# Optimization experiments

Measured on AMD Instinct MI355X. Metric: run time of the kernel, lower is better.

## Reference

```python
import jax, jax.numpy as jnp
import numpy as np

B, N, M = 8, 1024, 1024
D_MODEL, D_HEAD, M_BITS = 1024, 128, 32
SCALE = 1.0 / np.sqrt(M_BITS)


def setup_inputs() -> dict:
    key = jax.random.key(0)
    ks = jax.random.split(key, 11)
    w_std = 1.0 / np.sqrt(D_MODEL)  # ~ nn.Linear init scale
    f32 = jnp.float32
    return {
        "Q": jax.random.normal(ks[0], (B, N, D_MODEL), dtype=f32),
        "K": jax.random.normal(ks[1], (B, M, D_MODEL), dtype=f32),
        "V": jax.random.normal(ks[2], (B, M, D_MODEL), dtype=f32),
        "Wq_boolean": jax.random.normal(ks[3], (D_MODEL, M_BITS), dtype=f32) * w_std,
        "Wk_boolean": jax.random.normal(ks[4], (D_MODEL, M_BITS), dtype=f32) * w_std,
        "Wq_tropical": jax.random.normal(ks[5], (D_MODEL, M_BITS), dtype=f32) * w_std,
        "Wk_tropical": jax.random.normal(ks[6], (D_MODEL, M_BITS), dtype=f32) * w_std,
        "Wq_real": jax.random.normal(ks[7], (D_MODEL, M_BITS), dtype=f32) * w_std,
        "Wk_real": jax.random.normal(ks[8], (D_MODEL, M_BITS), dtype=f32) * w_std,
        "Wv": jax.random.normal(ks[9], (D_MODEL, D_HEAD), dtype=f32) * w_std,
        "fusion_weights": jnp.ones((3,), dtype=f32),
        "mask": jnp.ones((B, N, M), dtype=jnp.int32),
    }


def _tropical_sim(Qe, Ke):
    # max-plus (tropical) witness similarity: sim[b,n,m] = max_d (Qe[b,n,d] + Ke[b,m,d])
    # loop over the small fixed bit dim (M_BITS=32) to avoid a [B,N,M,M_BITS] tensor
    acc = Qe[:, :, 0][:, :, None] + Ke[:, :, 0][:, None, :]
    for b in range(1, M_BITS):
        acc = jnp.maximum(acc, Qe[:, :, b][:, :, None] + Ke[:, :, b][:, None, :])
    return acc  # [B,N,M]


def reference(Q, K, V, Wq_boolean, Wk_boolean, Wq_tropical, Wk_tropical,
              Wq_real, Wk_real, Wv, fusion_weights, mask):
    # --- boolean monoid: hard-binarized codes, bit-match count ---
    Qb = (Q @ Wq_boolean > 0).astype(Q.dtype)   # [B,N,m]
    Kb = (K @ Wk_boolean > 0).astype(K.dtype)   # [B,M,m]
    sim_bool = (jnp.einsum('bnd,bmd->bnm', Qb, Kb)
                + jnp.einsum('bnd,bmd->bnm', 1.0 - Qb, 1.0 - Kb))
    # --- tropical monoid: max-plus over continuous codes ---
    sim_trop = _tropical_sim(Q @ Wq_tropical, K @ Wk_tropical)
    # --- real monoid: inner product of continuous codes ---
    sim_real = jnp.einsum('bnd,bmd->bnm', Q @ Wq_real, K @ Wk_real)
    # --- learned fusion + scaled softmax attention ---
    w = jax.nn.softmax(fusion_weights)
    scores = (w[0] * sim_bool + w[1] * sim_trop + w[2] * sim_real) * SCALE
    scores = jnp.where(mask == 0, -jnp.inf, scores)
    attn = jax.nn.softmax(scores, axis=-1)     # [B,N,M]  (dropout: eval mode, identity)
    out = jnp.einsum('bnm,bmh->bnh', attn, V @ Wv)  # [B,N,d_head]
    return out, attn
```

## Files before the change

kernel.cpp:

```cpp
#include <hip/hip_runtime.h>
#include <stdint.h>
#include <math.h>


#define SCALE_F 0.17677669529663687f

typedef float4 f4;

__device__ __forceinline__ float f4c(const f4 v, int i) {
    return i == 0 ? v.x : (i == 1 ? v.y : (i == 2 ? v.z : v.w));
}


__global__ __launch_bounds__(256)
void proj_qk_kernel(const float* __restrict__ Q, const float* __restrict__ K,
                    const float* __restrict__ Wqb, const float* __restrict__ Wkb,
                    const float* __restrict__ Wqt, const float* __restrict__ Wkt,
                    const float* __restrict__ Wqr, const float* __restrict__ Wkr,
                    float* __restrict__ Pq, float* __restrict__ Pk) {
    const int t = threadIdx.x;
    const int bx = blockIdx.x;
    const int by = blockIdx.y;
    const int side = blockIdx.z;
    const float* __restrict__ X  = side ? K   : Q;
    const float* __restrict__ Wb = side ? Wkb : Wqb;
    const float* __restrict__ Wt = side ? Wkt : Wqt;
    const float* __restrict__ Wr = side ? Wkr : Wqr;
    float* __restrict__ P = side ? Pk : Pq;

    __shared__ float Xs[128][68];
    __shared__ float Ws[64][96];

    const int r0 = bx * 128;
    const int rt = t >> 3;
    const int cg = t & 7;

    float acc[4][12];
    #pragma unroll
    for (int i = 0; i < 4; ++i)
        #pragma unroll
        for (int j = 0; j < 12; ++j) acc[i][j] = 0.f;

    for (int dc = 0; dc < 4; ++dc) {
        const int dbase = by * 256 + dc * 64;
        #pragma unroll
        for (int k2 = 0; k2 < 8; ++k2) {
            int idx = t + k2 * 256;
            int r = idx >> 4, c4 = idx & 15;
            *(f4*)&Xs[r][c4 * 4] = *(const f4*)&X[(size_t)(r0 + r) * 1024 + dbase + c4 * 4];
        }
        #pragma unroll
        for (int k2 = 0; k2 < 6; ++k2) {
            int idx = t + k2 * 256;
            int d = idx / 24, c4 = idx % 24;
            const float* __restrict__ src = (c4 < 8) ? Wb : ((c4 < 16) ? Wt : Wr);
            *(f4*)&Ws[d][c4 * 4] = *(const f4*)&src[(size_t)(dbase + d) * 32 + (c4 & 7) * 4];
        }
        __syncthreads();
        for (int dd = 0; dd < 64; dd += 4) {
            f4 xf[4];
            #pragma unroll
            for (int i = 0; i < 4; ++i) xf[i] = *(const f4*)&Xs[4 * rt + i][dd];
            #pragma unroll
            for (int d2 = 0; d2 < 4; ++d2) {
                f4 wf[3];
                #pragma unroll
                for (int jj = 0; jj < 3; ++jj)
                    wf[jj] = *(const f4*)&Ws[dd + d2][12 * cg + 4 * jj];
                #pragma unroll
                for (int i = 0; i < 4; ++i) {
                    const float xv = f4c(xf[i], d2);
                    #pragma unroll
                    for (int jj = 0; jj < 3; ++jj) {
                        acc[i][jj * 4 + 0] += xv * wf[jj].x;
                        acc[i][jj * 4 + 1] += xv * wf[jj].y;
                        acc[i][jj * 4 + 2] += xv * wf[jj].z;
                        acc[i][jj * 4 + 3] += xv * wf[jj].w;
                    }
                }
            }
        }
        __syncthreads();
    }
    #pragma unroll
    for (int i = 0; i < 4; ++i) {
        size_t base = ((size_t)by * 8192 + r0 + 4 * rt + i) * 96 + 12 * cg;
        *(f4*)&P[base + 0] = make_float4(acc[i][0], acc[i][1], acc[i][2],  acc[i][3]);
        *(f4*)&P[base + 4] = make_float4(acc[i][4], acc[i][5], acc[i][6],  acc[i][7]);
        *(f4*)&P[base + 8] = make_float4(acc[i][8], acc[i][9], acc[i][10], acc[i][11]);
    }
}

__global__ __launch_bounds__(256)
void proj_v_kernel(const float* __restrict__ V, const float* __restrict__ Wv,
                   float* __restrict__ P) {
    const int t = threadIdx.x;
    const int r0 = blockIdx.x * 128;
    const int by = blockIdx.y;
    __shared__ float Xs[128][36];
    __shared__ float Ws[32][128];
    const int rt = t >> 3, cg = t & 7;

    float acc[4][16];
    #pragma unroll
    for (int i = 0; i < 4; ++i)
        #pragma unroll
        for (int j = 0; j < 16; ++j) acc[i][j] = 0.f;

    for (int dc = 0; dc < 8; ++dc) {
        const int dbase = by * 256 + dc * 32;
        #pragma unroll
        for (int k2 = 0; k2 < 4; ++k2) {
            int idx = t + k2 * 256;
            int r = idx >> 3, c4 = idx & 7;
            *(f4*)&Xs[r][c4 * 4] = *(const f4*)&V[(size_t)(r0 + r) * 1024 + dbase + c4 * 4];
        }
        #pragma unroll
        for (int k2 = 0; k2 < 4; ++k2) {
            int idx = t + k2 * 256;
            int d = idx >> 5, c4 = idx & 31;
            *(f4*)&Ws[d][c4 * 4] = *(const f4*)&Wv[(size_t)(dbase + d) * 128 + c4 * 4];
        }
        __syncthreads();
        for (int dd = 0; dd < 32; dd += 4) {
            f4 xf[4];
            #pragma unroll
            for (int i = 0; i < 4; ++i) xf[i] = *(const f4*)&Xs[4 * rt + i][dd];
            #pragma unroll
            for (int d2 = 0; d2 < 4; ++d2) {
                f4 wf[4];
                #pragma unroll
                for (int jj = 0; jj < 4; ++jj)
                    wf[jj] = *(const f4*)&Ws[dd + d2][16 * cg + 4 * jj];
                #pragma unroll
                for (int i = 0; i < 4; ++i) {
                    const float xv = f4c(xf[i], d2);
                    #pragma unroll
                    for (int jj = 0; jj < 4; ++jj) {
                        acc[i][jj * 4 + 0] += xv * wf[jj].x;
                        acc[i][jj * 4 + 1] += xv * wf[jj].y;
                        acc[i][jj * 4 + 2] += xv * wf[jj].z;
                        acc[i][jj * 4 + 3] += xv * wf[jj].w;
                    }
                }
            }
        }
        __syncthreads();
    }
    #pragma unroll
    for (int i = 0; i < 4; ++i) {
        size_t base = ((size_t)by * 8192 + r0 + 4 * rt + i) * 128 + 16 * cg;
        #pragma unroll
        for (int jj = 0; jj < 4; ++jj)
            *(f4*)&P[base + 4 * jj] = make_float4(acc[i][jj * 4 + 0], acc[i][jj * 4 + 1],
                                                  acc[i][jj * 4 + 2], acc[i][jj * 4 + 3]);
    }
}


__global__ __launch_bounds__(256)
void pack_codes_kernel(const float* __restrict__ Pq, const float* __restrict__ Pk,
                       float* __restrict__ Qt, float* __restrict__ Qr,
                       float* __restrict__ Kt, float* __restrict__ Kr) {
    const int gid = blockIdx.x * 256 + threadIdx.x;
    const int side = blockIdx.y;
    const float* __restrict__ P = side ? Pk : Pq;
    const int row = gid >> 6, c = gid & 63;
    float s = 0.f;
    #pragma unroll
    for (int g = 0; g < 4; ++g) s += P[((size_t)g * 8192 + row) * 96 + 32 + c];
    float* __restrict__ dT = side ? Kt : Qt;
    float* __restrict__ dR = side ? Kr : Qr;
    if (c < 32) dT[row * 32 + c] = s;
    else        dR[row * 32 + (c - 32)] = s;
}

__global__ __launch_bounds__(256)
void pack_bits_kernel(const float* __restrict__ Pq, const float* __restrict__ Pk,
                      uint32_t* __restrict__ Qbits, uint32_t* __restrict__ Kbits) {
    const int gid = blockIdx.x * 256 + threadIdx.x;
    const int side = blockIdx.y;
    const float* __restrict__ P = side ? Pk : Pq;
    const int row = gid >> 5, c = gid & 31;
    float s = 0.f;
    #pragma unroll
    for (int g = 0; g < 4; ++g) s += P[((size_t)g * 8192 + row) * 96 + c];
    const unsigned long long bm = __ballot(s > 0.f);
    uint32_t* __restrict__ bits = side ? Kbits : Qbits;
    const int lane = threadIdx.x & 63;
    if (lane == 0)       bits[row] = (uint32_t)bm;
    else if (lane == 32) bits[row] = (uint32_t)(bm >> 32);
}

__global__ __launch_bounds__(256)
void reduce4_kernel(const float* __restrict__ P, float* __restrict__ dst) {
    const int gid = blockIdx.x * 256 + threadIdx.x;
    f4 a = ((const f4*)P)[gid];
    f4 b = ((const f4*)P)[262144 + gid];
    f4 c = ((const f4*)P)[2 * 262144 + gid];
    f4 d = ((const f4*)P)[3 * 262144 + gid];
    ((f4*)dst)[gid] = make_float4(a.x + b.x + c.x + d.x, a.y + b.y + c.y + d.y,
                                  a.z + b.z + c.z + d.z, a.w + b.w + c.w + d.w);
}


__global__ __launch_bounds__(256)
void scores_kernel(const float* __restrict__ Qt, const float* __restrict__ Qr,
                   const float* __restrict__ Kt, const float* __restrict__ Kr,
                   const uint32_t* __restrict__ Qbits, const uint32_t* __restrict__ Kbits,
                   const float* __restrict__ fw, float* __restrict__ attn) {
    const int t = threadIdx.x;
    const int m0 = blockIdx.x * 64;
    const int n0 = blockIdx.y * 64;
    const int b  = blockIdx.z;

    __shared__ float Qt_s[64][36], Qr_s[64][36];
    __shared__ float KtT[32][68],  KrT[32][68];
    __shared__ uint32_t qb_s[64], kb_s[64];

    #pragma unroll
    for (int k2 = 0; k2 < 2; ++k2) {
        int idx = t + k2 * 256;
        int r = idx >> 3, c4 = idx & 7;
        *(f4*)&Qt_s[r][c4 * 4] = *(const f4*)&Qt[(size_t)(b * 1024 + n0 + r) * 32 + c4 * 4];
        *(f4*)&Qr_s[r][c4 * 4] = *(const f4*)&Qr[(size_t)(b * 1024 + n0 + r) * 32 + c4 * 4];
        f4 vt = *(const f4*)&Kt[(size_t)(b * 1024 + m0 + r) * 32 + c4 * 4];
        f4 vr = *(const f4*)&Kr[(size_t)(b * 1024 + m0 + r) * 32 + c4 * 4];
        KtT[c4 * 4 + 0][r] = vt.x; KtT[c4 * 4 + 1][r] = vt.y;
        KtT[c4 * 4 + 2][r] = vt.z; KtT[c4 * 4 + 3][r] = vt.w;
        KrT[c4 * 4 + 0][r] = vr.x; KrT[c4 * 4 + 1][r] = vr.y;
        KrT[c4 * 4 + 2][r] = vr.z; KrT[c4 * 4 + 3][r] = vr.w;
    }
    if (t < 64)       qb_s[t] = Qbits[b * 1024 + n0 + t];
    else if (t < 128) kb_s[t - 64] = Kbits[b * 1024 + m0 + (t - 64)];
    __syncthreads();

    const float f0 = fw[0], f1 = fw[1], f2 = fw[2];
    const float fm = fmaxf(f0, fmaxf(f1, f2));
    const float e0 = __expf(f0 - fm), e1 = __expf(f1 - fm), e2 = __expf(f2 - fm);
    const float wi = 1.f / (e0 + e1 + e2);
    const float w0 = e0 * wi, w1 = e1 * wi, w2 = e2 * wi;

    const int rg = t >> 4, mg = t & 15;

    float tacc[4][4], racc[4][4];
    #pragma unroll
    for (int i = 0; i < 4; ++i)
        #pragma unroll
        for (int j = 0; j < 4; ++j) { tacc[i][j] = -INFINITY; racc[i][j] = 0.f; }

    for (int d0 = 0; d0 < 32; d0 += 4) {
        f4 qt4[4], qr4[4];
        #pragma unroll
        for (int i = 0; i < 4; ++i) {
            qt4[i] = *(const f4*)&Qt_s[4 * rg + i][d0];
            qr4[i] = *(const f4*)&Qr_s[4 * rg + i][d0];
        }
        #pragma unroll
        for (int d2 = 0; d2 < 4; ++d2) {
            const f4 kt = *(const f4*)&KtT[d0 + d2][4 * mg];
            const f4 kr = *(const f4*)&KrT[d0 + d2][4 * mg];
            #pragma unroll
            for (int i = 0; i < 4; ++i) {
                const float qtv = f4c(qt4[i], d2);
                const float qrv = f4c(qr4[i], d2);
                tacc[i][0] = fmaxf(tacc[i][0], qtv + kt.x);
                tacc[i][1] = fmaxf(tacc[i][1], qtv + kt.y);
                tacc[i][2] = fmaxf(tacc[i][2], qtv + kt.z);
                tacc[i][3] = fmaxf(tacc[i][3], qtv + kt.w);
                racc[i][0] += qrv * kr.x;
                racc[i][1] += qrv * kr.y;
                racc[i][2] += qrv * kr.z;
                racc[i][3] += qrv * kr.w;
            }
        }
    }

    uint32_t qb[4], kb[4];
    #pragma unroll
    for (int i = 0; i < 4; ++i) { qb[i] = qb_s[4 * rg + i]; kb[i] = kb_s[4 * mg + i]; }
    #pragma unroll
    for (int i = 0; i < 4; ++i) {
        float sj[4];
        #pragma unroll
        for (int j = 0; j < 4; ++j) {
            const float cnt = (float)(32 - __popc(qb[i] ^ kb[j]));
            sj[j] = (w0 * cnt + w1 * tacc[i][j] + w2 * racc[i][j]) * SCALE_F;
        }
        *(f4*)&attn[(size_t)(b * 1024 + n0 + 4 * rg + i) * 1024 + m0 + 4 * mg] =
            make_float4(sj[0], sj[1], sj[2], sj[3]);
    }
}


__global__ __launch_bounds__(256)
void softmax_kernel(float* __restrict__ attn, const int* __restrict__ mask) {
    const int row = blockIdx.x;
    const int t = threadIdx.x;
    const f4  s4 = ((const f4*)attn)[(size_t)row * 256 + t];
    const int4 m4 = ((const int4*)mask)[(size_t)row * 256 + t];
    const float v0 = m4.x ? s4.x : -INFINITY;
    const float v1 = m4.y ? s4.y : -INFINITY;
    const float v2 = m4.z ? s4.z : -INFINITY;
    const float v3 = m4.w ? s4.w : -INFINITY;

    float tm = fmaxf(fmaxf(v0, v1), fmaxf(v2, v3));
    #pragma unroll
    for (int off = 32; off >= 1; off >>= 1) tm = fmaxf(tm, __shfl_xor(tm, off, 64));
    __shared__ float rmax[4], rsum[4];
    if ((t & 63) == 0) rmax[t >> 6] = tm;
    __syncthreads();
    const float gm = fmaxf(fmaxf(rmax[0], rmax[1]), fmaxf(rmax[2], rmax[3]));

    const float x0 = m4.x ? __expf(v0 - gm) : 0.f;
    const float x1 = m4.y ? __expf(v1 - gm) : 0.f;
    const float x2 = m4.z ? __expf(v2 - gm) : 0.f;
    const float x3 = m4.w ? __expf(v3 - gm) : 0.f;
    float ts = (x0 + x1) + (x2 + x3);
    #pragma unroll
    for (int off = 32; off >= 1; off >>= 1) ts += __shfl_xor(ts, off, 64);
    if ((t & 63) == 0) rsum[t >> 6] = ts;
    __syncthreads();
    const float inv = 1.f / (((rsum[0] + rsum[1]) + (rsum[2] + rsum[3])));

    ((f4*)attn)[(size_t)row * 256 + t] = make_float4(x0 * inv, x1 * inv, x2 * inv, x3 * inv);
}


__global__ __launch_bounds__(256)
void pv_kernel(const float* __restrict__ attn, const float* __restrict__ Vp,
               float* __restrict__ Pout) {
    const int t = threadIdx.x;
    const int row0 = blockIdx.x * 64;
    const int ms = blockIdx.y;
    const int b = row0 >> 10;
    __shared__ float As[64][68];
    __shared__ float Vs[64][128];
    const int rt = t >> 4, hg = t & 15;

    float acc[4][8];
    #pragma unroll
    for (int i = 0; i < 4; ++i)
        #pragma unroll
        for (int j = 0; j < 8; ++j) acc[i][j] = 0.f;

    for (int mc = 0; mc < 4; ++mc) {
        const int mb = ms * 256 + mc * 64;
        #pragma unroll
        for (int k2 = 0; k2 < 4; ++k2) {
            int idx = t + k2 * 256;
            int r = idx >> 4, c4 = idx & 15;
            *(f4*)&As[r][c4 * 4] = *(const f4*)&attn[(size_t)(row0 + r) * 1024 + mb + c4 * 4];
        }
        #pragma unroll
        for (int k2 = 0; k2 < 8; ++k2) {
            int idx = t + k2 * 256;
            int m = idx >> 5, c4 = idx & 31;
            *(f4*)&Vs[m][c4 * 4] = *(const f4*)&Vp[(size_t)(b * 1024 + mb + m) * 128 + c4 * 4];
        }
        __syncthreads();
        for (int m = 0; m < 64; ++m) {
            const f4 u0 = *(const f4*)&Vs[m][hg * 8];
            const f4 u1 = *(const f4*)&Vs[m][hg * 8 + 4];
            #pragma unroll
            for (int i = 0; i < 4; ++i) {
                const float a = As[4 * rt + i][m];
                acc[i][0] += a * u0.x; acc[i][1] += a * u0.y;
                acc[i][2] += a * u0.z; acc[i][3] += a * u0.w;
                acc[i][4] += a * u1.x; acc[i][5] += a * u1.y;
                acc[i][6] += a * u1.z; acc[i][7] += a * u1.w;
            }
        }
        __syncthreads();
    }
    #pragma unroll
    for (int i = 0; i < 4; ++i) {
        size_t base = ((size_t)ms * 8192 + row0 + 4 * rt + i) * 128 + hg * 8;
        *(f4*)&Pout[base]     = make_float4(acc[i][0], acc[i][1], acc[i][2], acc[i][3]);
        *(f4*)&Pout[base + 4] = make_float4(acc[i][4], acc[i][5], acc[i][6], acc[i][7]);
    }
}


extern "C" void kernel_launch(void* const* d_in, const int* in_sizes, int n_in,
                              void* d_out, int out_size, void* d_ws, size_t ws_size,
                              hipStream_t stream) {
    const float* Q   = (const float*)d_in[0];
    const float* K   = (const float*)d_in[1];
    const float* V   = (const float*)d_in[2];
    const float* Wqb = (const float*)d_in[3];
    const float* Wkb = (const float*)d_in[4];
    const float* Wqt = (const float*)d_in[5];
    const float* Wkt = (const float*)d_in[6];
    const float* Wqr = (const float*)d_in[7];
    const float* Wkr = (const float*)d_in[8];
    const float* Wv  = (const float*)d_in[9];
    const float* fw  = (const float*)d_in[10];
    const int*  mask = (const int*)d_in[11];

    float* ws = (float*)d_ws;
    float* Qt = ws;
    float* Qr = Qt + 262144;
    float* Kt = Qr + 262144;
    float* Kr = Kt + 262144;
    float* Vp = Kr + 262144;
    uint32_t* Qbits = (uint32_t*)(Vp + 1048576);
    uint32_t* Kbits = Qbits + 8192;
    float* Pbig = (float*)(Kbits + 8192);

    float* out  = (float*)d_out;
    float* attn = out + 1048576;
    float* Pq = attn;
    float* Pk = attn + 3145728;

    proj_qk_kernel<<<dim3(64, 4, 2), 256, 0, stream>>>(Q, K, Wqb, Wkb, Wqt, Wkt, Wqr, Wkr, Pq, Pk);
    proj_v_kernel<<<dim3(64, 4), 256, 0, stream>>>(V, Wv, Pbig);
    pack_codes_kernel<<<dim3(2048, 2), 256, 0, stream>>>(Pq, Pk, Qt, Qr, Kt, Kr);
    pack_bits_kernel<<<dim3(1024, 2), 256, 0, stream>>>(Pq, Pk, Qbits, Kbits);
    reduce4_kernel<<<1024, 256, 0, stream>>>(Pbig, Vp);
    scores_kernel<<<dim3(16, 16, 8), 256, 0, stream>>>(Qt, Qr, Kt, Kr, Qbits, Kbits, fw, attn);
    softmax_kernel<<<8192, 256, 0, stream>>>(attn, mask);
    pv_kernel<<<dim3(128, 4), 256, 0, stream>>>(attn, Vp, Pbig);
    reduce4_kernel<<<1024, 256, 0, stream>>>(Pbig, out);
}
```

Baseline: 313.7 us.

## Rewrite pipeline on bf16 split-precision MFMA with packed f16 tropical max-plus

```diff
diff --git a/kernel.cpp b/kernel.cpp
--- a/kernel.cpp
+++ b/kernel.cpp
@@ -1,4 +1,5 @@
 #include <hip/hip_runtime.h>
+#include <hip/hip_fp16.h>
 #include <stdint.h>
 #include <math.h>
 
@@ -6,305 +7,377 @@
 #define SCALE_F 0.17677669529663687f
 
 typedef float4 f4;
-
+typedef unsigned int uint_t;
+typedef __attribute__((ext_vector_type(8))) short s16x8;
+typedef __attribute__((ext_vector_type(8))) unsigned short u16x8;
+typedef __attribute__((ext_vector_type(4))) float f32x4;
+
+__device__ __forceinline__ unsigned short f2bf(float x) {
+    unsigned u = __float_as_uint(x);
+    return (unsigned short)((u + 0x7FFFu + ((u >> 16) & 1u)) >> 16);
+}
+__device__ __forceinline__ float bf2f(unsigned short h) {
+    return __uint_as_float(((unsigned)h) << 16);
+}
 __device__ __forceinline__ float f4c(const f4 v, int i) {
     return i == 0 ? v.x : (i == 1 ? v.y : (i == 2 ? v.z : v.w));
 }
+__device__ __forceinline__ unsigned pk_add(unsigned a, unsigned b) {
+    unsigned r;
+    asm("v_pk_add_f16 %0, %1, %2" : "=v"(r) : "v"(a), "v"(b));
+    return r;
+}
+__device__ __forceinline__ unsigned pk_max(unsigned a, unsigned b) {
+    unsigned r;
+    asm("v_pk_max_f16 %0, %1, %2" : "=v"(r) : "v"(a), "v"(b));
+    return r;
+}
+__device__ __forceinline__ float h2f(unsigned short u) {
+    __half h;
+    *reinterpret_cast<unsigned short*>(&h) = u;
+    return __half2float(h);
+}
+__device__ __forceinline__ unsigned short f2h(float x) {
+    __half h = __float2half(x);
+    return *reinterpret_cast<unsigned short*>(&h);
+}
+
+#define MFMA16(a, b, c) __builtin_amdgcn_mfma_f32_16x16x32_bf16((a), (b), (c), 0, 0, 0)
 
 
 __global__ __launch_bounds__(256)
-void proj_qk_kernel(const float* __restrict__ Q, const float* __restrict__ K,
-                    const float* __restrict__ Wqb, const float* __restrict__ Wkb,
-                    const float* __restrict__ Wqt, const float* __restrict__ Wkt,
-                    const float* __restrict__ Wqr, const float* __restrict__ Wkr,
-                    float* __restrict__ Pq, float* __restrict__ Pk) {
+void conv_w_kernel(const float* __restrict__ Wqb, const float* __restrict__ Wkb,
+                   const float* __restrict__ Wqt, const float* __restrict__ Wkt,
+                   const float* __restrict__ Wqr, const float* __restrict__ Wkr,
+                   const float* __restrict__ Wv,
+                   unsigned short* __restrict__ Wh, unsigned short* __restrict__ Wm,
+                   unsigned short* __restrict__ Wl3,
+                   unsigned short* __restrict__ Wvh, unsigned short* __restrict__ Wvm) {
+    __shared__ float T[256][33];
     const int t = threadIdx.x;
+    const int bid = blockIdx.x;
+    const float* src;
+    int kb, outRowBase, srcStride, srcColBase, side = 0;
+    bool isQK, isBool;
+    if (bid < 24) {
+        side = bid / 12;
+        int cb = (bid % 12) / 4;
+        kb = bid & 3;
+        const float* mats[6] = {Wqb, Wqt, Wqr, Wkb, Wkt, Wkr};
+        src = mats[side * 3 + cb];
+        srcStride = 32; srcColBase = 0;
+        outRowBase = side * 96 + cb * 32;
+        isQK = true; isBool = (cb == 0);
+    } else {
+        int v = bid - 24;
+        int hb = v >> 2; kb = v & 3;
+        src = Wv; srcStride = 128; srcColBase = hb * 32;
+        outRowBase = hb * 32;
+        isQK = false; isBool = false;
+    }
+    #pragma unroll
+    for (int i = 0; i < 8; ++i) {
+        int idx = t + i * 256;
+        int r = idx >> 3, c4 = idx & 7;
+        f4 v = *(const f4*)&src[(size_t)(kb * 256 + r) * srcStride + srcColBase + c4 * 4];
+        T[r][c4 * 4 + 0] = v.x; T[r][c4 * 4 + 1] = v.y;
+        T[r][c4 * 4 + 2] = v.z; T[r][c4 * 4 + 3] = v.w;
+    }
+    __syncthreads();
+    const int col = t >> 3, kseg = t & 7;
+    unsigned short* dh = isQK ? Wh : Wvh;
+    unsigned short* dm = isQK ? Wm : Wvm;
+    size_t obase = (size_t)(outRowBase + col) * 1024 + kb * 256 + kseg * 32;
+    u16x8 ph[4], pm[4], pl[4];
+    #pragma unroll
+    for (int i = 0; i < 32; ++i) {
+        float x = T[kseg * 32 + i][col];
+        unsigned short hb_ = f2bf(x);
+        float r1 = x - bf2f(hb_);
+        unsigned short mb_ = f2bf(r1);
+        float r2 = r1 - bf2f(mb_);
+        ph[i >> 3][i & 7] = hb_;
+        pm[i >> 3][i & 7] = mb_;
+        pl[i >> 3][i & 7] = f2bf(r2);
+    }
+    #pragma unroll
+    for (int i = 0; i < 4; ++i) {
+        *(u16x8*)&dh[obase + i * 8] = ph[i];
+        *(u16x8*)&dm[obase + i * 8] = pm[i];
+    }
+    if (isBool) {
+        size_t lbase = (size_t)(side * 32 + col) * 1024 + kb * 256 + kseg * 32;
+        #pragma unroll
+        for (int i = 0; i < 4; ++i) *(u16x8*)&Wl3[lbase + i * 8] = pl[i];
+    }
+}
+
+
+__global__ __launch_bounds__(256)
+void proj_kernel(const float* __restrict__ Q, const float* __restrict__ K,
+                 const float* __restrict__ V,
+                 const unsigned short* __restrict__ Wh, const unsigned short* __restrict__ Wm,
+                 const unsigned short* __restrict__ Wl3,
+                 const unsigned short* __restrict__ Wvh, const unsigned short* __restrict__ Wvm,
+                 unsigned short* __restrict__ Qt_q, unsigned short* __restrict__ Kt_q,
+                 unsigned short* __restrict__ Qrh, unsigned short* __restrict__ Qrm,
+                 unsigned short* __restrict__ Krh, unsigned short* __restrict__ Krm,
+                 uint_t* __restrict__ Qbits, uint_t* __restrict__ Kbits,
+                 unsigned short* __restrict__ VphT, unsigned short* __restrict__ VpmT) {
+    __shared__ unsigned short BH[16384], BM[16384], BL[4096];
+    __shared__ uint_t sb[64];
+    const int t = threadIdx.x, lane = t & 63, w = t >> 6;
+    const int g = lane >> 4, l15 = lane & 15;
     const int bx = blockIdx.x;
-    const int by = blockIdx.y;
-    const int side = blockIdx.z;
-    const float* __restrict__ X  = side ? K   : Q;
-    const float* __restrict__ Wb = side ? Wkb : Wqb;
-    const float* __restrict__ Wt = side ? Wkt : Wqt;
-    const float* __restrict__ Wr = side ? Wkr : Wqr;
-    float* __restrict__ P = side ? Pk : Pq;
-
-    __shared__ float Xs[128][68];
-    __shared__ float Ws[64][96];
-
-    const int r0 = bx * 128;
-    const int rt = t >> 3;
-    const int cg = t & 7;
-
-    float acc[4][12];
-    #pragma unroll
-    for (int i = 0; i < 4; ++i)
-        #pragma unroll
-        for (int j = 0; j < 12; ++j) acc[i][j] = 0.f;
-
-    for (int dc = 0; dc < 4; ++dc) {
-        const int dbase = by * 256 + dc * 64;
-        #pragma unroll
-        for (int k2 = 0; k2 < 8; ++k2) {
-            int idx = t + k2 * 256;
-            int r = idx >> 4, c4 = idx & 15;
-            *(f4*)&Xs[r][c4 * 4] = *(const f4*)&X[(size_t)(r0 + r) * 1024 + dbase + c4 * 4];
-        }
-        #pragma unroll
-        for (int k2 = 0; k2 < 6; ++k2) {
-            int idx = t + k2 * 256;
-            int d = idx / 24, c4 = idx % 24;
-            const float* __restrict__ src = (c4 < 8) ? Wb : ((c4 < 16) ? Wt : Wr);
-            *(f4*)&Ws[d][c4 * 4] = *(const f4*)&src[(size_t)(dbase + d) * 32 + (c4 & 7) * 4];
+    const bool isV = bx >= 256;
+    const int side = isV ? 2 : (bx >> 7);
+    const int tile = isV ? (bx - 256) : (bx & 127);
+    const float* __restrict__ X = (side == 0) ? Q : (side == 1 ? K : V);
+    const int row0 = isV ? tile * 32 : tile * 64;
+    const int rowh = isV ? (w & 1) * 16 : w * 16;
+    const int hbase = isV ? (w >> 1) * 64 : 0;
+    const int arowg = row0 + rowh + l15;
+    const float* __restrict__ Xrow = X + (size_t)arowg * 1024;
+
+    if (t < 64) sb[t] = 0;
+
+    f32x4 acc[8];
+    #pragma unroll
+    for (int i = 0; i < 8; ++i) acc[i] = f32x4{0.f, 0.f, 0.f, 0.f};
+
+    for (int c = 0; c < 8; ++c) {
+        const int k0 = c * 128;
+        f4 ar[8];
+        #pragma unroll
+        for (int ks = 0; ks < 4; ++ks) {
+            ar[2 * ks]     = *(const f4*)&Xrow[k0 + ks * 32 + g * 8];
+            ar[2 * ks + 1] = *(const f4*)&Xrow[k0 + ks * 32 + g * 8 + 4];
         }
         __syncthreads();
-        for (int dd = 0; dd < 64; dd += 4) {
-            f4 xf[4];
-            #pragma unroll
-            for (int i = 0; i < 4; ++i) xf[i] = *(const f4*)&Xs[4 * rt + i][dd];
-            #pragma unroll
-            for (int d2 = 0; d2 < 4; ++d2) {
-                f4 wf[3];
+        if (!isV) {
+            #pragma unroll
+            for (int i = 0; i < 14; ++i) {
+                int s = t + i * 256;
+                int col, ks; const unsigned short* src; char* dp;
+                if (s < 1536)      { col = s >> 4; ks = s & 15;
+                    src = &Wh[(size_t)(side * 96 + col) * 1024 + k0 + ks * 8]; dp = (char*)BH; }
+                else if (s < 3072) { int s2 = s - 1536; col = s2 >> 4; ks = s2 & 15;
+                    src = &Wm[(size_t)(side * 96 + col) * 1024 + k0 + ks * 8]; dp = (char*)BM; }
+                else               { int s2 = s - 3072; col = s2 >> 4; ks = s2 & 15;
+                    src = &Wl3[(size_t)(side * 32 + col) * 1024 + k0 + ks * 8]; dp = (char*)BL; }
+                u16x8 v = *(const u16x8*)src;
+                *(u16x8*)(dp + col * 256 + ((ks * 16) ^ ((col & 7) << 4))) = v;
+            }
+        } else {
+            #pragma unroll
+            for (int i = 0; i < 16; ++i) {
+                int s = t + i * 256;
+                int col, ks; const unsigned short* src; char* dp;
+                if (s < 2048) { col = s >> 4; ks = s & 15;
+                    src = &Wvh[(size_t)col * 1024 + k0 + ks * 8]; dp = (char*)BH; }
+                else          { int s2 = s - 2048; col = s2 >> 4; ks = s2 & 15;
+                    src = &Wvm[(size_t)col * 1024 + k0 + ks * 8]; dp = (char*)BM; }
+                u16x8 v = *(const u16x8*)src;
+                *(u16x8*)(dp + col * 256 + ((ks * 16) ^ ((col & 7) << 4))) = v;
+            }
+        }
+        __syncthreads();
+
+        #pragma unroll
+        for (int ks = 0; ks < 4; ++ks) {
+            u16x8 ah, am, al;
+            #pragma unroll
+            for (int j = 0; j < 8; ++j) {
+                float x = (j < 4) ? f4c(ar[2 * ks], j) : f4c(ar[2 * ks + 1], j - 4);
+                unsigned short hb_ = f2bf(x);
+                float r1 = x - bf2f(hb_);
+                unsigned short mb_ = f2bf(r1);
+                ah[j] = hb_; am[j] = mb_;
+                al[j] = f2bf(r1 - bf2f(mb_));
+            }
+            s16x8 a1 = (s16x8)ah, a2 = (s16x8)am;
+            const int kbyte = (ks * 4 + g) * 16;
+            if (!isV) {
+                s16x8 a3 = (s16x8)al;
                 #pragma unroll
-                for (int jj = 0; jj < 3; ++jj)
-                    wf[jj] = *(const f4*)&Ws[dd + d2][12 * cg + 4 * jj];
+                for (int cf = 0; cf < 2; ++cf) {
+                    int col = cf * 16 + l15;
+                    int off = col * 256 + (kbyte ^ ((col & 7) << 4));
+                    s16x8 bh = *(s16x8*)((char*)BH + off);
+                    s16x8 bm = *(s16x8*)((char*)BM + off);
+                    s16x8 bl = *(s16x8*)((char*)BL + off);
+                    acc[cf] = MFMA16(a1, bh, acc[cf]);
+                    acc[cf] = MFMA16(a1, bm, acc[cf]);
+                    acc[cf] = MFMA16(a2, bh, acc[cf]);
+                    acc[cf] = MFMA16(a2, bm, acc[cf]);
+                    acc[cf] = MFMA16(a3, bh, acc[cf]);
+                }
                 #pragma unroll
-                for (int i = 0; i < 4; ++i) {
-                    const float xv = f4c(xf[i], d2);
+                for (int cf = 2; cf < 4; ++cf) {
+                    int col = cf * 16 + l15;
+                    int off = col * 256 + (kbyte ^ ((col & 7) << 4));
+                    s16x8 bh = *(s16x8*)((char*)BH + off);
+                    acc[cf] = MFMA16(a1, bh, acc[cf]);
+                }
+                #pragma unroll
+                for (int cf = 4; cf < 6; ++cf) {
+                    int col = cf * 16 + l15;
+                    int off = col * 256 + (kbyte ^ ((col & 7) << 4));
+                    s16x8 bh = *(s16x8*)((char*)BH + off);
+                    s16x8 bm = *(s16x8*)((char*)BM + off);
+                    acc[cf] = MFMA16(a1, bh, acc[cf]);
+                    acc[cf] = MFMA16(a1, bm, acc[cf]);
+                    acc[cf] = MFMA16(a2, bh, acc[cf]);
+                }
+            } else {
+                #pragma unroll
+                for (int cf = 0; cf < 4; ++cf) {
+                    int col = hbase + cf * 16 + l15;
+                    int off = col * 256 + (kbyte ^ ((col & 7) << 4));
+                    s16x8 bh = *(s16x8*)((char*)BH + off);
+                    s16x8 bm = *(s16x8*)((char*)BM + off);
+                    acc[cf] = MFMA16(a1, bh, acc[cf]);
+                    acc[cf] = MFMA16(a1, bm, acc[cf]);
+                    acc[cf] = MFMA16(a2, bh, acc[cf]);
+                }
+            }
+        }
+    }
+
+    if (!isV) {
+        #pragma unroll
+        for (int cf = 0; cf < 2; ++cf)
+            #pragma unroll
+            for (int r = 0; r < 4; ++r) {
+                unsigned long long bm = __ballot(acc[cf][r] > 0.f);
+                if (lane == 0) {
                     #pragma unroll
-                    for (int jj = 0; jj < 3; ++jj) {
-                        acc[i][jj * 4 + 0] += xv * wf[jj].x;
-                        acc[i][jj * 4 + 1] += xv * wf[jj].y;
-                        acc[i][jj * 4 + 2] += xv * wf[jj].z;
-                        acc[i][jj * 4 + 3] += xv * wf[jj].w;
-                    }
+                    for (int gg = 0; gg < 4; ++gg)
+                        sb[w * 16 + gg * 4 + r] |=
+                            (uint_t)((bm >> (16 * gg)) & 0xFFFFull) << (16 * cf);
                 }
             }
-        }
+        unsigned short* Tt = side ? Kt_q : Qt_q;
+        unsigned short* Rh = side ? Krh : Qrh;
+        unsigned short* Rm = side ? Krm : Qrm;
+        #pragma unroll
+        for (int cf = 2; cf < 4; ++cf)
+            #pragma unroll
+            for (int r = 0; r < 4; ++r) {
+                int grow = row0 + w * 16 + g * 4 + r;
+                int tcol = (cf - 2) * 16 + l15;
+                Tt[(size_t)grow * 32 + tcol] = f2h(acc[cf][r]);
+            }
+        #pragma unroll
+        for (int cf = 4; cf < 6; ++cf)
+            #pragma unroll
+            for (int r = 0; r < 4; ++r) {
+                int grow = row0 + w * 16 + g * 4 + r;
+                int rcol = (cf - 4) * 16 + l15;
+                float v = acc[cf][r];
+                unsigned short h = f2bf(v);
+                Rh[(size_t)grow * 32 + rcol] = h;
+                Rm[(size_t)grow * 32 + rcol] = f2bf(v - bf2f(h));
+            }
         __syncthreads();
-    }
-    #pragma unroll
-    for (int i = 0; i < 4; ++i) {
-        size_t base = ((size_t)by * 8192 + r0 + 4 * rt + i) * 96 + 12 * cg;
-        *(f4*)&P[base + 0] = make_float4(acc[i][0], acc[i][1], acc[i][2],  acc[i][3]);
-        *(f4*)&P[base + 4] = make_float4(acc[i][4], acc[i][5], acc[i][6],  acc[i][7]);
-        *(f4*)&P[base + 8] = make_float4(acc[i][8], acc[i][9], acc[i][10], acc[i][11]);
-    }
-}
+        uint_t* Tb = side ? Kbits : Qbits;
+        if (t < 64) Tb[row0 + t] = sb[t];
+    } else {
+        const int b = tile >> 5;
+        const int mbase = (tile & 31) * 32 + (w & 1) * 16 + g * 4;
+        #pragma unroll
+        for (int cf = 0; cf < 4; ++cf) {
+            int colh = hbase + cf * 16 + l15;
+            ushort4 hv, mv;
+            float v0 = acc[cf][0], v1 = acc[cf][1], v2 = acc[cf][2], v3 = acc[cf][3];
+            unsigned short h0 = f2bf(v0), h1 = f2bf(v1), h2_ = f2bf(v2), h3 = f2bf(v3);
+            hv = make_ushort4(h0, h1, h2_, h3);
+            mv = make_ushort4(f2bf(v0 - bf2f(h0)), f2bf(v1 - bf2f(h1)),
+                              f2bf(v2 - bf2f(h2_)), f2bf(v3 - bf2f(h3)));
+            size_t ob = (size_t)(b * 128 + colh) * 1024 + mbase;
+            *(ushort4*)&VphT[ob] = hv;
+            *(ushort4*)&VpmT[ob] = mv;
+        }
+    }
+}
+
 
 __global__ __launch_bounds__(256)
-void proj_v_kernel(const float* __restrict__ V, const float* __restrict__ Wv,
-                   float* __restrict__ P) {
-    const int t = threadIdx.x;
-    const int r0 = blockIdx.x * 128;
-    const int by = blockIdx.y;
-    __shared__ float Xs[128][36];
-    __shared__ float Ws[32][128];
-    const int rt = t >> 3, cg = t & 7;
-
-    float acc[4][16];
-    #pragma unroll
-    for (int i = 0; i < 4; ++i)
-        #pragma unroll
-        for (int j = 0; j < 16; ++j) acc[i][j] = 0.f;
-
-    for (int dc = 0; dc < 8; ++dc) {
-        const int dbase = by * 256 + dc * 32;
-        #pragma unroll
-        for (int k2 = 0; k2 < 4; ++k2) {
-            int idx = t + k2 * 256;
-            int r = idx >> 3, c4 = idx & 7;
-            *(f4*)&Xs[r][c4 * 4] = *(const f4*)&V[(size_t)(r0 + r) * 1024 + dbase + c4 * 4];
-        }
-        #pragma unroll
-        for (int k2 = 0; k2 < 4; ++k2) {
-            int idx = t + k2 * 256;
-            int d = idx >> 5, c4 = idx & 31;
-            *(f4*)&Ws[d][c4 * 4] = *(const f4*)&Wv[(size_t)(dbase + d) * 128 + c4 * 4];
-        }
-        __syncthreads();
-        for (int dd = 0; dd < 32; dd += 4) {
-            f4 xf[4];
-            #pragma unroll
-            for (int i = 0; i < 4; ++i) xf[i] = *(const f4*)&Xs[4 * rt + i][dd];
-            #pragma unroll
-            for (int d2 = 0; d2 < 4; ++d2) {
-                f4 wf[4];
-                #pragma unroll
-                for (int jj = 0; jj < 4; ++jj)
-                    wf[jj] = *(const f4*)&Ws[dd + d2][16 * cg + 4 * jj];
-                #pragma unroll
-                for (int i = 0; i < 4; ++i) {
-                    const float xv = f4c(xf[i], d2);
-                    #pragma unroll
-                    for (int jj = 0; jj < 4; ++jj) {
-                        acc[i][jj * 4 + 0] += xv * wf[jj].x;
-                        acc[i][jj * 4 + 1] += xv * wf[jj].y;
-                        acc[i][jj * 4 + 2] += xv * wf[jj].z;
-                        acc[i][jj * 4 + 3] += xv * wf[jj].w;
-                    }
-                }
-            }
-        }
-        __syncthreads();
-    }
-    #pragma unroll
-    for (int i = 0; i < 4; ++i) {
-        size_t base = ((size_t)by * 8192 + r0 + 4 * rt + i) * 128 + 16 * cg;
-        #pragma unroll
-        for (int jj = 0; jj < 4; ++jj)
-            *(f4*)&P[base + 4 * jj] = make_float4(acc[i][jj * 4 + 0], acc[i][jj * 4 + 1],
-                                                  acc[i][jj * 4 + 2], acc[i][jj * 4 + 3]);
-    }
-}
-
-
-__global__ __launch_bounds__(256)
-void pack_codes_kernel(const float* __restrict__ Pq, const float* __restrict__ Pk,
-                       float* __restrict__ Qt, float* __restrict__ Qr,
-                       float* __restrict__ Kt, float* __restrict__ Kr) {
-    const int gid = blockIdx.x * 256 + threadIdx.x;
-    const int side = blockIdx.y;
-    const float* __restrict__ P = side ? Pk : Pq;
-    const int row = gid >> 6, c = gid & 63;
-    float s = 0.f;
-    #pragma unroll
-    for (int g = 0; g < 4; ++g) s += P[((size_t)g * 8192 + row) * 96 + 32 + c];
-    float* __restrict__ dT = side ? Kt : Qt;
-    float* __restrict__ dR = side ? Kr : Qr;
-    if (c < 32) dT[row * 32 + c] = s;
-    else        dR[row * 32 + (c - 32)] = s;
-}
-
-__global__ __launch_bounds__(256)
-void pack_bits_kernel(const float* __restrict__ Pq, const float* __restrict__ Pk,
-                      uint32_t* __restrict__ Qbits, uint32_t* __restrict__ Kbits) {
-    const int gid = blockIdx.x * 256 + threadIdx.x;
-    const int side = blockIdx.y;
-    const float* __restrict__ P = side ? Pk : Pq;
-    const int row = gid >> 5, c = gid & 31;
-    float s = 0.f;
-    #pragma unroll
-    for (int g = 0; g < 4; ++g) s += P[((size_t)g * 8192 + row) * 96 + c];
-    const unsigned long long bm = __ballot(s > 0.f);
-    uint32_t* __restrict__ bits = side ? Kbits : Qbits;
-    const int lane = threadIdx.x & 63;
-    if (lane == 0)       bits[row] = (uint32_t)bm;
-    else if (lane == 32) bits[row] = (uint32_t)(bm >> 32);
-}
-
-__global__ __launch_bounds__(256)
-void reduce4_kernel(const float* __restrict__ P, float* __restrict__ dst) {
-    const int gid = blockIdx.x * 256 + threadIdx.x;
-    f4 a = ((const f4*)P)[gid];
-    f4 b = ((const f4*)P)[262144 + gid];
-    f4 c = ((const f4*)P)[2 * 262144 + gid];
-    f4 d = ((const f4*)P)[3 * 262144 + gid];
-    ((f4*)dst)[gid] = make_float4(a.x + b.x + c.x + d.x, a.y + b.y + c.y + d.y,
-                                  a.z + b.z + c.z + d.z, a.w + b.w + c.w + d.w);
-}
-
-
-__global__ __launch_bounds__(256)
-void scores_kernel(const float* __restrict__ Qt, const float* __restrict__ Qr,
-                   const float* __restrict__ Kt, const float* __restrict__ Kr,
-                   const uint32_t* __restrict__ Qbits, const uint32_t* __restrict__ Kbits,
-                   const float* __restrict__ fw, float* __restrict__ attn) {
-    const int t = threadIdx.x;
-    const int m0 = blockIdx.x * 64;
-    const int n0 = blockIdx.y * 64;
-    const int b  = blockIdx.z;
-
-    __shared__ float Qt_s[64][36], Qr_s[64][36];
-    __shared__ float KtT[32][68],  KrT[32][68];
-    __shared__ uint32_t qb_s[64], kb_s[64];
-
-    #pragma unroll
-    for (int k2 = 0; k2 < 2; ++k2) {
-        int idx = t + k2 * 256;
-        int r = idx >> 3, c4 = idx & 7;
-        *(f4*)&Qt_s[r][c4 * 4] = *(const f4*)&Qt[(size_t)(b * 1024 + n0 + r) * 32 + c4 * 4];
-        *(f4*)&Qr_s[r][c4 * 4] = *(const f4*)&Qr[(size_t)(b * 1024 + n0 + r) * 32 + c4 * 4];
-        f4 vt = *(const f4*)&Kt[(size_t)(b * 1024 + m0 + r) * 32 + c4 * 4];
-        f4 vr = *(const f4*)&Kr[(size_t)(b * 1024 + m0 + r) * 32 + c4 * 4];
-        KtT[c4 * 4 + 0][r] = vt.x; KtT[c4 * 4 + 1][r] = vt.y;
-        KtT[c4 * 4 + 2][r] = vt.z; KtT[c4 * 4 + 3][r] = vt.w;
-        KrT[c4 * 4 + 0][r] = vr.x; KrT[c4 * 4 + 1][r] = vr.y;
-        KrT[c4 * 4 + 2][r] = vr.z; KrT[c4 * 4 + 3][r] = vr.w;
-    }
-    if (t < 64)       qb_s[t] = Qbits[b * 1024 + n0 + t];
-    else if (t < 128) kb_s[t - 64] = Kbits[b * 1024 + m0 + (t - 64)];
-    __syncthreads();
-
+void scores_kernel(const unsigned short* __restrict__ Qt_q, const unsigned short* __restrict__ Kt_q,
+                   const unsigned short* __restrict__ Qrh, const unsigned short* __restrict__ Qrm,
+                   const unsigned short* __restrict__ Krh, const unsigned short* __restrict__ Krm,
+                   const uint_t* __restrict__ Qbits, const uint_t* __restrict__ Kbits,
+                   const int* __restrict__ mask, const float* __restrict__ fw,
+                   float* __restrict__ attn) {
+    const int t = threadIdx.x, lane = t & 63, w = t >> 6;
+    const int g = lane >> 4, l15 = lane & 15;
+    const int b = blockIdx.y, n0 = blockIdx.x * 16;
+    const int rowA = b * 1024 + n0;
+
+    s16x8 qrh = *(const s16x8*)&Qrh[(size_t)(rowA + l15) * 32 + g * 8];
+    s16x8 qrm = *(const s16x8*)&Qrm[(size_t)(rowA + l15) * 32 + g * 8];
+    uint_t qt[4][16], qb[4];
+    #pragma unroll
+    for (int r = 0; r < 4; ++r) {
+        const uint_t* p = (const uint_t*)&Qt_q[(size_t)(rowA + 4 * g + r) * 32];
+        #pragma unroll
+        for (int j = 0; j < 16; ++j) qt[r][j] = p[j];
+        qb[r] = Qbits[rowA + 4 * g + r];
+    }
     const float f0 = fw[0], f1 = fw[1], f2 = fw[2];
     const float fm = fmaxf(f0, fmaxf(f1, f2));
     const float e0 = __expf(f0 - fm), e1 = __expf(f1 - fm), e2 = __expf(f2 - fm);
     const float wi = 1.f / (e0 + e1 + e2);
     const float w0 = e0 * wi, w1 = e1 * wi, w2 = e2 * wi;
 
-    const int rg = t >> 4, mg = t & 15;
-
-    float tacc[4][4], racc[4][4];
-    #pragma unroll
-    for (int i = 0; i < 4; ++i)
-        #pragma unroll
-        for (int j = 0; j < 4; ++j) { tacc[i][j] = -INFINITY; racc[i][j] = 0.f; }
-
-    for (int d0 = 0; d0 < 32; d0 += 4) {
-        f4 qt4[4], qr4[4];
-        #pragma unroll
-        for (int i = 0; i < 4; ++i) {
-            qt4[i] = *(const f4*)&Qt_s[4 * rg + i][d0];
-            qr4[i] = *(const f4*)&Qr_s[4 * rg + i][d0];
-        }
-        #pragma unroll
-        for (int d2 = 0; d2 < 4; ++d2) {
-            const f4 kt = *(const f4*)&KtT[d0 + d2][4 * mg];
-            const f4 kr = *(const f4*)&KrT[d0 + d2][4 * mg];
-            #pragma unroll
-            for (int i = 0; i < 4; ++i) {
-                const float qtv = f4c(qt4[i], d2);
-                const float qrv = f4c(qr4[i], d2);
-                tacc[i][0] = fmaxf(tacc[i][0], qtv + kt.x);
-                tacc[i][1] = fmaxf(tacc[i][1], qtv + kt.y);
-                tacc[i][2] = fmaxf(tacc[i][2], qtv + kt.z);
-                tacc[i][3] = fmaxf(tacc[i][3], qtv + kt.w);
-                racc[i][0] += qrv * kr.x;
-                racc[i][1] += qrv * kr.y;
-                racc[i][2] += qrv * kr.z;
-                racc[i][3] += qrv * kr.w;
-            }
-        }
-    }
-
-    uint32_t qb[4], kb[4];
-    #pragma unroll
-    for (int i = 0; i < 4; ++i) { qb[i] = qb_s[4 * rg + i]; kb[i] = kb_s[4 * mg + i]; }
-    #pragma unroll
-    for (int i = 0; i < 4; ++i) {
-        float sj[4];
-        #pragma unroll
-        for (int j = 0; j < 4; ++j) {
-            const float cnt = (float)(32 - __popc(qb[i] ^ kb[j]));
-            sj[j] = (w0 * cnt + w1 * tacc[i][j] + w2 * racc[i][j]) * SCALE_F;
-        }
-        *(f4*)&attn[(size_t)(b * 1024 + n0 + 4 * rg + i) * 1024 + m0 + 4 * mg] =
-            make_float4(sj[0], sj[1], sj[2], sj[3]);
+    for (int i = 0; i < 16; ++i) {
+        const int m0 = (w + 4 * i) * 16;
+        const int mrow = b * 1024 + m0;
+        const uint_t* ktp = (const uint_t*)&Kt_q[(size_t)(mrow + l15) * 32];
+        uint_t kt[16];
+        #pragma unroll
+        for (int j = 0; j < 16; ++j) kt[j] = ktp[j];
+        s16x8 krh = *(const s16x8*)&Krh[(size_t)(mrow + l15) * 32 + g * 8];
+        s16x8 krm = *(const s16x8*)&Krm[(size_t)(mrow + l15) * 32 + g * 8];
+        uint_t kb = Kbits[mrow + l15];
+        int mk[4];
+        #pragma unroll
+        for (int r = 0; r < 4; ++r)
+            mk[r] = mask[(size_t)(rowA + 4 * g + r) * 1024 + m0 + l15];
+
+        f32x4 rc = f32x4{0.f, 0.f, 0.f, 0.f};
+        rc = MFMA16(qrh, krh, rc);
+        rc = MFMA16(qrh, krm, rc);
+        rc = MFMA16(qrm, krh, rc);
+
+        float trop[4];
+        #pragma unroll
+        for (int r = 0; r < 4; ++r) {
+            unsigned a = pk_add(qt[r][0], kt[0]);
+            #pragma unroll
+            for (int j = 1; j < 16; ++j)
+                a = pk_max(a, pk_add(qt[r][j], kt[j]));
+            trop[r] = fmaxf(h2f((unsigned short)(a & 0xFFFF)),
+                            h2f((unsigned short)(a >> 16)));
+        }
+        #pragma unroll
+        for (int r = 0; r < 4; ++r) {
+            float cnt = (float)(32 - __popc(qb[r] ^ kb));
+            float s = (w0 * cnt + w1 * trop[r] + w2 * rc[r]) * SCALE_F;
+            s = mk[r] ? s : -INFINITY;
+            attn[(size_t)(rowA + 4 * g + r) * 1024 + m0 + l15] = s;
+        }
     }
 }
 
 
 __global__ __launch_bounds__(256)
-void softmax_kernel(float* __restrict__ attn, const int* __restrict__ mask) {
+void softmax_kernel(float* __restrict__ attn) {
     const int row = blockIdx.x;
     const int t = threadIdx.x;
-    const f4  s4 = ((const f4*)attn)[(size_t)row * 256 + t];
-    const int4 m4 = ((const int4*)mask)[(size_t)row * 256 + t];
-    const float v0 = m4.x ? s4.x : -INFINITY;
-    const float v1 = m4.y ? s4.y : -INFINITY;
-    const float v2 = m4.z ? s4.z : -INFINITY;
-    const float v3 = m4.w ? s4.w : -INFINITY;
-
-    float tm = fmaxf(fmaxf(v0, v1), fmaxf(v2, v3));
+    const f4 s4 = ((const f4*)attn)[(size_t)row * 256 + t];
+
+    float tm = fmaxf(fmaxf(s4.x, s4.y), fmaxf(s4.z, s4.w));
     #pragma unroll
     for (int off = 32; off >= 1; off >>= 1) tm = fmaxf(tm, __shfl_xor(tm, off, 64));
     __shared__ float rmax[4], rsum[4];
@@ -312,73 +385,88 @@
     __syncthreads();
     const float gm = fmaxf(fmaxf(rmax[0], rmax[1]), fmaxf(rmax[2], rmax[3]));
 
-    const float x0 = m4.x ? __expf(v0 - gm) : 0.f;
-    const float x1 = m4.y ? __expf(v1 - gm) : 0.f;
-    const float x2 = m4.z ? __expf(v2 - gm) : 0.f;
-    const float x3 = m4.w ? __expf(v3 - gm) : 0.f;
+    const float x0 = __expf(s4.x - gm);
+    const float x1 = __expf(s4.y - gm);
+    const float x2 = __expf(s4.z - gm);
+    const float x3 = __expf(s4.w - gm);
     float ts = (x0 + x1) + (x2 + x3);
     #pragma unroll
     for (int off = 32; off >= 1; off >>= 1) ts += __shfl_xor(ts, off, 64);
     if ((t & 63) == 0) rsum[t >> 6] = ts;
     __syncthreads();
-    const float inv = 1.f / (((rsum[0] + rsum[1]) + (rsum[2] + rsum[3])));
+    const float inv = 1.f / ((rsum[0] + rsum[1]) + (rsum[2] + rsum[3]));
 
     ((f4*)attn)[(size_t)row * 256 + t] = make_float4(x0 * inv, x1 * inv, x2 * inv, x3 * inv);
 }
 
 
 __global__ __launch_bounds__(256)
-void pv_kernel(const float* __restrict__ attn, const float* __restrict__ Vp,
-               float* __restrict__ Pout) {
-    const int t = threadIdx.x;
-    const int row0 = blockIdx.x * 64;
-    const int ms = blockIdx.y;
-    const int b = row0 >> 10;
-    __shared__ float As[64][68];
-    __shared__ float Vs[64][128];
-    const int rt = t >> 4, hg = t & 15;
-
-    float acc[4][8];
-    #pragma unroll
-    for (int i = 0; i < 4; ++i)
-        #pragma unroll
-        for (int j = 0; j < 8; ++j) acc[i][j] = 0.f;
-
-    for (int mc = 0; mc < 4; ++mc) {
-        const int mb = ms * 256 + mc * 64;
-        #pragma unroll
-        for (int k2 = 0; k2 < 4; ++k2) {
-            int idx = t + k2 * 256;
-            int r = idx >> 4, c4 = idx & 15;
-            *(f4*)&As[r][c4 * 4] = *(const f4*)&attn[(size_t)(row0 + r) * 1024 + mb + c4 * 4];
-        }
-        #pragma unroll
-        for (int k2 = 0; k2 < 8; ++k2) {
-            int idx = t + k2 * 256;
-            int m = idx >> 5, c4 = idx & 31;
-            *(f4*)&Vs[m][c4 * 4] = *(const f4*)&Vp[(size_t)(b * 1024 + mb + m) * 128 + c4 * 4];
+void pv_kernel(const float* __restrict__ attn,
+               const unsigned short* __restrict__ VphT, const unsigned short* __restrict__ VpmT,
+               float* __restrict__ out) {
+    __shared__ unsigned short BH[16384], BM[16384];
+    const int t = threadIdx.x, lane = t & 63, w = t >> 6;
+    const int g = lane >> 4, l15 = lane & 15;
+    const int b = blockIdx.y, n0 = blockIdx.x * 32;
+    const int rowh = (w & 1) * 16;
+    const int hbase = (w >> 1) * 64;
+    const float* __restrict__ Arow = attn + (size_t)(b * 1024 + n0 + rowh + l15) * 1024;
+
+    f32x4 acc[4];
+    #pragma unroll
+    for (int i = 0; i < 4; ++i) acc[i] = f32x4{0.f, 0.f, 0.f, 0.f};
+
+    for (int c = 0; c < 8; ++c) {
+        const int m0 = c * 128;
+        f4 ar[8];
+        #pragma unroll
+        for (int ks = 0; ks < 4; ++ks) {
+            ar[2 * ks]     = *(const f4*)&Arow[m0 + ks * 32 + g * 8];
+            ar[2 * ks + 1] = *(const f4*)&Arow[m0 + ks * 32 + g * 8 + 4];
         }
         __syncthreads();
-        for (int m = 0; m < 64; ++m) {
-            const f4 u0 = *(const f4*)&Vs[m][hg * 8];
-            const f4 u1 = *(const f4*)&Vs[m][hg * 8 + 4];
-            #pragma unroll
-            for (int i = 0; i < 4; ++i) {
-                const float a = As[4 * rt + i][m];
-                acc[i][0] += a * u0.x; acc[i][1] += a * u0.y;
-                acc[i][2] += a * u0.z; acc[i][3] += a * u0.w;
-                acc[i][4] += a * u1.x; acc[i][5] += a * u1.y;
-                acc[i][6] += a * u1.z; acc[i][7] += a * u1.w;
-            }
+        #pragma unroll
+        for (int i = 0; i < 16; ++i) {
+            int s = t + i * 256;
+            int col, ks; const unsigned short* src; char* dp;
+            if (s < 2048) { col = s >> 4; ks = s & 15;
+                src = &VphT[(size_t)(b * 128 + col) * 1024 + m0 + ks * 8]; dp = (char*)BH; }
+            else          { int s2 = s - 2048; col = s2 >> 4; ks = s2 & 15;
+                src = &VpmT[(size_t)(b * 128 + col) * 1024 + m0 + ks * 8]; dp = (char*)BM; }
+            u16x8 v = *(const u16x8*)src;
+            *(u16x8*)(dp + col * 256 + ((ks * 16) ^ ((col & 7) << 4))) = v;
         }
         __syncthreads();
-    }
-    #pragma unroll
-    for (int i = 0; i < 4; ++i) {
-        size_t base = ((size_t)ms * 8192 + row0 + 4 * rt + i) * 128 + hg * 8;
-        *(f4*)&Pout[base]     = make_float4(acc[i][0], acc[i][1], acc[i][2], acc[i][3]);
-        *(f4*)&Pout[base + 4] = make_float4(acc[i][4], acc[i][5], acc[i][6], acc[i][7]);
-    }
+
+        #pragma unroll
+        for (int ks = 0; ks < 4; ++ks) {
+            u16x8 ah, am;
+            #pragma unroll
+            for (int j = 0; j < 8; ++j) {
+                float x = (j < 4) ? f4c(ar[2 * ks], j) : f4c(ar[2 * ks + 1], j - 4);
+                unsigned short hb_ = f2bf(x);
+                ah[j] = hb_; am[j] = f2bf(x - bf2f(hb_));
+            }
+            s16x8 a1 = (s16x8)ah, a2 = (s16x8)am;
+            const int kbyte = (ks * 4 + g) * 16;
+            #pragma unroll
+            for (int cf = 0; cf < 4; ++cf) {
+                int col = hbase + cf * 16 + l15;
+                int off = col * 256 + (kbyte ^ ((col & 7) << 4));
+                s16x8 bh = *(s16x8*)((char*)BH + off);
+                s16x8 bm = *(s16x8*)((char*)BM + off);
+                acc[cf] = MFMA16(a1, bh, acc[cf]);
+                acc[cf] = MFMA16(a1, bm, acc[cf]);
+                acc[cf] = MFMA16(a2, bh, acc[cf]);
+            }
+        }
+    }
+    #pragma unroll
+    for (int cf = 0; cf < 4; ++cf)
+        #pragma unroll
+        for (int r = 0; r < 4; ++r)
+            out[(size_t)(b * 1024 + n0 + rowh + g * 4 + r) * 128 + hbase + cf * 16 + l15] =
+                acc[cf][r];
 }
 
 
@@ -398,28 +486,33 @@
     const float* fw  = (const float*)d_in[10];
     const int*  mask = (const int*)d_in[11];
 
-    float* ws = (float*)d_ws;
-    float* Qt = ws;
-    float* Qr = Qt + 262144;
-    float* Kt = Qr + 262144;
-    float* Kr = Kt + 262144;
-    float* Vp = Kr + 262144;
-    uint32_t* Qbits = (uint32_t*)(Vp + 1048576);
-    uint32_t* Kbits = Qbits + 8192;
-    float* Pbig = (float*)(Kbits + 8192);
+    unsigned short* wsu = (unsigned short*)d_ws;
+    unsigned short* Wh   = wsu;
+    unsigned short* Wm   = Wh + 196608;
+    unsigned short* Wl3  = Wm + 196608;
+    unsigned short* Wvh  = Wl3 + 65536;
+    unsigned short* Wvm  = Wvh + 131072;
+    unsigned short* Qt_q = Wvm + 131072;
+    unsigned short* Kt_q = Qt_q + 262144;
+    unsigned short* Qrh  = Kt_q + 262144;
+    unsigned short* Qrm  = Qrh + 262144;
+    unsigned short* Krh  = Qrm + 262144;
+    unsigned short* Krm  = Krh + 262144;
+    unsigned short* VphT = Krm + 262144;
+    unsigned short* VpmT = VphT + 1048576;
+    uint_t* Qbits = (uint_t*)(VpmT + 1048576);
+    uint_t* Kbits = Qbits + 8192;
 
     float* out  = (float*)d_out;
     float* attn = out + 1048576;
-    float* Pq = attn;
-    float* Pk = attn + 3145728;
-
-    proj_qk_kernel<<<dim3(64, 4, 2), 256, 0, stream>>>(Q, K, Wqb, Wkb, Wqt, Wkt, Wqr, Wkr, Pq, Pk);
-    proj_v_kernel<<<dim3(64, 4), 256, 0, stream>>>(V, Wv, Pbig);
-    pack_codes_kernel<<<dim3(2048, 2), 256, 0, stream>>>(Pq, Pk, Qt, Qr, Kt, Kr);
-    pack_bits_kernel<<<dim3(1024, 2), 256, 0, stream>>>(Pq, Pk, Qbits, Kbits);
-    reduce4_kernel<<<1024, 256, 0, stream>>>(Pbig, Vp);
-    scores_kernel<<<dim3(16, 16, 8), 256, 0, stream>>>(Qt, Qr, Kt, Kr, Qbits, Kbits, fw, attn);
-    softmax_kernel<<<8192, 256, 0, stream>>>(attn, mask);
-    pv_kernel<<<dim3(128, 4), 256, 0, stream>>>(attn, Vp, Pbig);
-    reduce4_kernel<<<1024, 256, 0, stream>>>(Pbig, out);
-}
+
+    conv_w_kernel<<<40, 256, 0, stream>>>(Wqb, Wkb, Wqt, Wkt, Wqr, Wkr, Wv,
+                                          Wh, Wm, Wl3, Wvh, Wvm);
+    proj_kernel<<<512, 256, 0, stream>>>(Q, K, V, Wh, Wm, Wl3, Wvh, Wvm,
+                                         Qt_q, Kt_q, Qrh, Qrm, Krh, Krm,
+                                         Qbits, Kbits, VphT, VpmT);
+    scores_kernel<<<dim3(64, 8), 256, 0, stream>>>(Qt_q, Kt_q, Qrh, Qrm, Krh, Krm,
+                                                   Qbits, Kbits, mask, fw, attn);
+    softmax_kernel<<<8192, 256, 0, stream>>>(attn);
+    pv_kernel<<<dim3(32, 8), 256, 0, stream>>>(attn, VphT, VpmT, out);
+}
```

Result: faster. 278.8 us (-11.1%).
